# Kernel optimization log

Measured on AMD Instinct MI355X. Metric: run time of the kernel, lower is better.

Reference implementation:

```python
import jax, jax.numpy as jnp
import numpy as np


def setup_inputs() -> dict:
    key = jax.random.key(0)
    ks = jax.random.split(key, 5)
    B, H, S, D = 4, 16, 2048, 64
    queries = jax.random.normal(ks[0], (B, H, S, D), dtype=jnp.float32)
    keys = jax.random.normal(ks[1], (B, H, S, D), dtype=jnp.float32)
    values = jax.random.normal(ks[2], (B, H, S, D), dtype=jnp.float32)
    W_out = jax.random.normal(ks[3], (D, D), dtype=jnp.float32) / np.sqrt(D)
    b_out = jax.random.normal(ks[4], (D,), dtype=jnp.float32) * 0.01
    return {"queries": queries, "keys": keys, "values": values, "W_out": W_out, "b_out": b_out}


def reference(queries, keys, values, W_out, b_out):
    # scores: [B,H,S,S] = Q K^T / sqrt(D)
    scale = 1.0 / np.sqrt(queries.shape[-1]).astype(np.float32)
    scores = jnp.einsum("bhqd,bhkd->bhqk", queries, keys) * scale
    # concrete attention distribution: softmax over keys axis
    distr = jax.nn.softmax(scores, axis=-1)
    # weighted sum of values: [B,H,S,D]
    out = jnp.einsum("bhqk,bhkd->bhqd", distr, values)
    # out projection (nn.Linear: x @ W^T + b)
    out = jnp.einsum("bhqd,ed->bhqe", out, W_out) + b_out
    return out
```

## Files before the change

kernel.cpp:

```cpp
#include <hip/hip_runtime.h>
#include <math.h>


typedef __attribute__((ext_vector_type(8)))  short    s16x8;
typedef __attribute__((ext_vector_type(4)))  float    f32x4;
typedef __attribute__((ext_vector_type(16))) float    f32x16;
typedef __attribute__((ext_vector_type(4)))  unsigned u32x4;

#define KQSCALE 0.18033688011112042f

__device__ __forceinline__ unsigned short f2bu(float x) {
    __bf16 v = (__bf16)x;
    return __builtin_bit_cast(unsigned short, v);
}
__device__ __forceinline__ short f2b(float x) { return (short)f2bu(x); }
__device__ __forceinline__ float b2f(short s) {
    __bf16 v = __builtin_bit_cast(__bf16, (unsigned short)s);
    return (float)v;
}
__device__ __forceinline__ unsigned pack2(float lo, float hi) {
    return (unsigned)f2bu(lo) | ((unsigned)f2bu(hi) << 16);
}
__device__ __forceinline__ int swzK(int row) { return (row & 7) << 4; }
__device__ __forceinline__ int swzV(int row) { return (((row >> 4) & 3) ^ (row & 7)) << 4; }

#define PLSWAP(x, y) asm("v_permlane32_swap_b32 %0, %1" : "+v"(x), "+v"(y))

#define BARRIER()                                              \
    do {                                                       \
        asm volatile("s_waitcnt lgkmcnt(0)" ::: "memory");     \
        __builtin_amdgcn_s_barrier();                          \
    } while (0)

#define WAVE_LDS_FENCE()                                       \
    do {                                                       \
        asm volatile("s_waitcnt lgkmcnt(0)" ::: "memory");     \
        __builtin_amdgcn_sched_barrier(0);                     \
    } while (0)

#define QK2(SA, SB, KsC, KT)                                                    \
    f32x16 SA = {}; f32x16 SB = {};                                             \
    __builtin_amdgcn_s_setprio(1);                                              \
    _Pragma("unroll")                                                           \
    for (int dt = 0; dt < 4; ++dt) {                                            \
        const int krow = (KT) * 32 + q32;                                       \
        s16x8 kf = *(s16x8*)((KsC) + krow * 128 +                               \
                             ((dt * 32 + h * 16) ^ swzK(krow)));                \
        SA = __builtin_amdgcn_mfma_f32_32x32x16_bf16(kf, qfA[dt], SA, 0, 0, 0); \
        SB = __builtin_amdgcn_mfma_f32_32x32x16_bf16(kf, qfB[dt], SB, 0, 0, 0); \
    }                                                                           \
    __builtin_amdgcn_s_setprio(0);

#define PVQ2(SA, SB, VtC, KT, T)                                               \
    do {                                                                       \
        const float ea0 = __builtin_amdgcn_exp2f((SA)[8 * (T) + 0]);           \
        const float ea1 = __builtin_amdgcn_exp2f((SA)[8 * (T) + 1]);           \
        const float ea2 = __builtin_amdgcn_exp2f((SA)[8 * (T) + 2]);           \
        const float ea3 = __builtin_amdgcn_exp2f((SA)[8 * (T) + 3]);           \
        const float ea4 = __builtin_amdgcn_exp2f((SA)[8 * (T) + 4]);           \
        const float ea5 = __builtin_amdgcn_exp2f((SA)[8 * (T) + 5]);           \
        const float ea6 = __builtin_amdgcn_exp2f((SA)[8 * (T) + 6]);           \
        const float ea7 = __builtin_amdgcn_exp2f((SA)[8 * (T) + 7]);           \
        const float eb0 = __builtin_amdgcn_exp2f((SB)[8 * (T) + 0]);           \
        const float eb1 = __builtin_amdgcn_exp2f((SB)[8 * (T) + 1]);           \
        const float eb2 = __builtin_amdgcn_exp2f((SB)[8 * (T) + 2]);           \
        const float eb3 = __builtin_amdgcn_exp2f((SB)[8 * (T) + 3]);           \
        const float eb4 = __builtin_amdgcn_exp2f((SB)[8 * (T) + 4]);           \
        const float eb5 = __builtin_amdgcn_exp2f((SB)[8 * (T) + 5]);           \
        const float eb6 = __builtin_amdgcn_exp2f((SB)[8 * (T) + 6]);           \
        const float eb7 = __builtin_amdgcn_exp2f((SB)[8 * (T) + 7]);           \
        unsigned ka0 = pack2(ea0, ea1), ka1 = pack2(ea2, ea3);                 \
        unsigned ka2 = pack2(ea4, ea5), ka3 = pack2(ea6, ea7);                 \
        PLSWAP(ka0, ka2);                                                      \
        PLSWAP(ka1, ka3);                                                      \
        u32x4 pwA; pwA[0] = ka0; pwA[1] = ka1; pwA[2] = ka2; pwA[3] = ka3;     \
        const s16x8 pA_ = __builtin_bit_cast(s16x8, pwA);                      \
        unsigned kb0 = pack2(eb0, eb1), kb1 = pack2(eb2, eb3);                 \
        unsigned kb2 = pack2(eb4, eb5), kb3 = pack2(eb6, eb7);                 \
        PLSWAP(kb0, kb2);                                                      \
        PLSWAP(kb1, kb3);                                                      \
        u32x4 pwB; pwB[0] = kb0; pwB[1] = kb1; pwB[2] = kb2; pwB[3] = kb3;     \
        const s16x8 pB_ = __builtin_bit_cast(s16x8, pwB);                      \
        const int kbo = (KT) * 64 + (T) * 32 + h * 16;                         \
        __builtin_amdgcn_s_setprio(1);                                         \
        s16x8 vf0 = *(s16x8*)((VtC) + q32 * 128 + (kbo ^ swzV(q32)));          \
        s16x8 vf1 = *(s16x8*)((VtC) + (32 + q32) * 128 + (kbo ^ swzV(32 + q32))); \
        accA0 = __builtin_amdgcn_mfma_f32_32x32x16_bf16(pA_, vf0, accA0, 0, 0, 0); \
        accB0 = __builtin_amdgcn_mfma_f32_32x32x16_bf16(pB_, vf0, accB0, 0, 0, 0); \
        accA1 = __builtin_amdgcn_mfma_f32_32x32x16_bf16(pA_, vf1, accA1, 0, 0, 0); \
        accB1 = __builtin_amdgcn_mfma_f32_32x32x16_bf16(pB_, vf1, accB1, 0, 0, 0); \
        rsA = __builtin_amdgcn_mfma_f32_32x32x16_bf16(pA_, onesV, rsA, 0, 0, 0); \
        rsB = __builtin_amdgcn_mfma_f32_32x32x16_bf16(pB_, onesV, rsB, 0, 0, 0); \
        __builtin_amdgcn_s_setprio(0);                                         \
    } while (0)

__global__ __launch_bounds__(512) void attn_fused(
    const float* __restrict__ Qg, const float* __restrict__ Kg,
    const float* __restrict__ Vg, const float* __restrict__ Wg,
    const float* __restrict__ bg, float* __restrict__ outg)
{
    __shared__ __align__(16) char smem[65536];
    char* KsB0 = smem;
    char* VtB0 = smem + 8192;
    char* KsB1 = smem + 16384;
    char* VtB1 = smem + 24576;
    char* KsB2 = smem + 32768;
    char* VtB2 = smem + 40960;
    char* KsB3 = smem + 49152;
    char* VtB3 = smem + 57344;

    const int tid  = threadIdx.x;
    const int wave = tid >> 6;
    const int lane = tid & 63;
    const int h    = lane >> 5;
    const int q32  = lane & 31;
    const int g    = lane >> 4;
    const int c    = lane & 15;

    const int orig = blockIdx.x;
    const int wg   = (orig & 7) * 32 + (orig >> 3);
    const int bh   = wg >> 2;
    const int qblk = wg & 3;

    const float* Qh = Qg + (size_t)bh * (2048 * 64);
    const float* Kh = Kg + (size_t)bh * (2048 * 64);
    const float* Vh = Vg + (size_t)bh * (2048 * 64);
    float*       Oh = outg + (size_t)bh * (2048 * 64);

    const int qbaseA = qblk * 512 + wave * 32;
    const int qbaseB = qbaseA + 256;

    const int srow = tid >> 3;
    const int scb  = (tid & 7) * 8;
    const int vk   = (tid >> 4) * 2;
    const int vd4  = (tid & 15) * 4;
    const int kOff = srow * 64 + scb;
    const int vOff = vk * 64 + vd4;

    f32x4 qLa[4], qLb[4], qLc[4], qLd[4];
#pragma unroll
    for (int dt = 0; dt < 4; ++dt) {
        const float* sA = Qh + (size_t)(qbaseA + q32) * 64 + dt * 16 + h * 8;
        const float* sB = Qh + (size_t)(qbaseB + q32) * 64 + dt * 16 + h * 8;
        qLa[dt] = *(const f32x4*)(sA);
        qLb[dt] = *(const f32x4*)(sA + 4);
        qLc[dt] = *(const f32x4*)(sB);
        qLd[dt] = *(const f32x4*)(sB + 4);
    }

    f32x4 rK0, rK1;
    f32x4 rV0, rV1;

    auto issueK = [&](int chunk) {
        const float* p = Kh + (size_t)chunk * 4096 + kOff;
        rK0 = *(const f32x4*)(p);
        rK1 = *(const f32x4*)(p + 4);
    };
    auto issueV = [&](int chunk) {
        const float* p = Vh + (size_t)chunk * 4096 + vOff;
        rV0 = *(const f32x4*)(p);
        rV1 = *(const f32x4*)(p + 64);
    };
    auto stageK = [&](char* KsD) {
        u32x4 wA;
        wA[0] = pack2(rK0[0], rK0[1]); wA[1] = pack2(rK0[2], rK0[3]);
        wA[2] = pack2(rK1[0], rK1[1]); wA[3] = pack2(rK1[2], rK1[3]);
        *(u32x4*)(KsD + srow * 128 + ((scb * 2) ^ swzK(srow))) = wA;
    };
    auto stageV = [&](char* VtD) {
#pragma unroll
        for (int i = 0; i < 4; ++i) {
            const int d = vd4 + i;
            *(unsigned*)(VtD + d * 128 + ((2 * vk) ^ swzV(d))) = pack2(rV0[i], rV1[i]);
        }
    };

    s16x8 qfA[4], qfB[4];
#pragma unroll
    for (int dt = 0; dt < 4; ++dt) {
        u32x4 fA, fB;
        fA[0] = pack2(qLa[dt][0] * KQSCALE, qLa[dt][1] * KQSCALE);
        fA[1] = pack2(qLa[dt][2] * KQSCALE, qLa[dt][3] * KQSCALE);
        fA[2] = pack2(qLb[dt][0] * KQSCALE, qLb[dt][1] * KQSCALE);
        fA[3] = pack2(qLb[dt][2] * KQSCALE, qLb[dt][3] * KQSCALE);
        fB[0] = pack2(qLc[dt][0] * KQSCALE, qLc[dt][1] * KQSCALE);
        fB[1] = pack2(qLc[dt][2] * KQSCALE, qLc[dt][3] * KQSCALE);
        fB[2] = pack2(qLd[dt][0] * KQSCALE, qLd[dt][1] * KQSCALE);
        fB[3] = pack2(qLd[dt][2] * KQSCALE, qLd[dt][3] * KQSCALE);
        qfA[dt] = __builtin_bit_cast(s16x8, fA);
        qfB[dt] = __builtin_bit_cast(s16x8, fB);
    }

    f32x16 accA0 = {}, accA1 = {}, accB0 = {}, accB1 = {};
    f32x16 rsA = {}, rsB = {};
    u32x4 onesW;
    onesW[0] = 0x3F803F80u; onesW[1] = 0x3F803F80u;
    onesW[2] = 0x3F803F80u; onesW[3] = 0x3F803F80u;
    const s16x8 onesV = __builtin_bit_cast(s16x8, onesW);

    auto one_iter = [&](char* KsC, char* VtC, char* KsS, char* VtS, int kc) {
        QK2(s0A, s0B, KsC, 0);
        PVQ2(s0A, s0B, VtC, 0, 0);
        if (kc <= 29) {
            stageK(KsS);
            if (kc <= 28) issueK(kc + 3);
        }
        PVQ2(s0A, s0B, VtC, 0, 1);
        QK2(s1A, s1B, KsC, 1);
        PVQ2(s1A, s1B, VtC, 1, 0);
        if (kc <= 29) {
            stageV(VtS);
            if (kc <= 28) issueV(kc + 3);
        }
        PVQ2(s1A, s1B, VtC, 1, 1);
    };

    issueK(0); issueV(0);
    stageK(KsB0); stageV(VtB0);
    issueK(1); issueV(1);
    stageK(KsB1); stageV(VtB1);
    issueK(2); issueV(2);
    BARRIER();

    for (int kc = 0; kc < 32; kc += 4) {
        one_iter(KsB0, VtB0, KsB2, VtB2, kc);
        one_iter(KsB1, VtB1, KsB3, VtB3, kc + 1);
        BARRIER();
        one_iter(KsB2, VtB2, KsB0, VtB0, kc + 2);
        one_iter(KsB3, VtB3, KsB1, VtB1, kc + 3);
        BARRIER();
    }

#pragma unroll
    for (int r = 0; r < 16; ++r) {
        const float ivA = __builtin_amdgcn_rcpf(rsA[r]);
        const float ivB = __builtin_amdgcn_rcpf(rsB[r]);
        accA0[r] *= ivA;  accA1[r] *= ivA;
        accB0[r] *= ivB;  accB1[r] *= ivB;
    }

    auto stageO = [&](const f32x16& a0, const f32x16& a1) {
        char* Ow = smem + wave * 8192;
#pragma unroll
        for (int r = 0; r < 16; ++r) {
            const int row = (r & 3) + 8 * (r >> 2) + 4 * h;
            const int sw  = (row & 7) << 5;
            *(float*)(Ow + row * 256 + ((q32 * 4)       ^ sw)) = a0[r];
            *(float*)(Ow + row * 256 + ((128 + q32 * 4) ^ sw)) = a1[r];
        }
    };
    auto project = [&](int qb) {
        char* Ow = smem + wave * 8192;
        f32x4 po[2][4];
#pragma unroll
        for (int rt = 0; rt < 2; ++rt)
#pragma unroll
            for (int et = 0; et < 4; ++et) {
                po[rt][et][0] = 0.f; po[rt][et][1] = 0.f;
                po[rt][et][2] = 0.f; po[rt][et][3] = 0.f;
            }
#pragma unroll
        for (int kh = 0; kh < 2; ++kh) {
            s16x8 ahi[2], alo[2];
#pragma unroll
            for (int rt = 0; rt < 2; ++rt) {
                const int row = rt * 16 + c;
                const int rb  = row * 256;
                const int rsw = (row & 7) << 5;
                const int o0  = (kh * 128 + g * 32) ^ rsw;
                f32x4 x0 = *(f32x4*)(Ow + rb + o0);
                f32x4 x1 = *(f32x4*)(Ow + rb + o0 + 16);
                s16x8 hh8, lo8;
#pragma unroll
                for (int j = 0; j < 4; ++j) {
                    const short hv = f2b(x0[j]);
                    hh8[j] = hv;  lo8[j] = f2b(x0[j] - b2f(hv));
                }
#pragma unroll
                for (int j = 0; j < 4; ++j) {
                    const short hv = f2b(x1[j]);
                    hh8[4 + j] = hv;  lo8[4 + j] = f2b(x1[j] - b2f(hv));
                }
                ahi[rt] = hh8; alo[rt] = lo8;
            }
#pragma unroll
            for (int et = 0; et < 4; ++et) {
                const float* ws = Wg + (et * 16 + c) * 64 + kh * 32 + g * 8;
                f32x4 w0 = *(const f32x4*)ws;
                f32x4 w1 = *(const f32x4*)(ws + 4);
                s16x8 whi, wlo;
#pragma unroll
                for (int j = 0; j < 4; ++j) {
                    const short hv = f2b(w0[j]);
                    whi[j] = hv;  wlo[j] = f2b(w0[j] - b2f(hv));
                }
#pragma unroll
                for (int j = 0; j < 4; ++j) {
                    const short hv = f2b(w1[j]);
                    whi[4 + j] = hv;  wlo[4 + j] = f2b(w1[j] - b2f(hv));
                }
#pragma unroll
                for (int rt = 0; rt < 2; ++rt) {
                    po[rt][et] = __builtin_amdgcn_mfma_f32_16x16x32_bf16(ahi[rt], whi, po[rt][et], 0, 0, 0);
                    po[rt][et] = __builtin_amdgcn_mfma_f32_16x16x32_bf16(alo[rt], whi, po[rt][et], 0, 0, 0);
                    po[rt][et] = __builtin_amdgcn_mfma_f32_16x16x32_bf16(ahi[rt], wlo, po[rt][et], 0, 0, 0);
                }
            }
        }
#pragma unroll
        for (int et = 0; et < 4; ++et) {
            const float bb = bg[et * 16 + c];
#pragma unroll
            for (int rt = 0; rt < 2; ++rt)
#pragma unroll
                for (int r = 0; r < 4; ++r) {
                    const int qrow = qb + rt * 16 + 4 * g + r;
                    Oh[(size_t)qrow * 64 + et * 16 + c] = po[rt][et][r] + bb;
                }
        }
    };

    stageO(accA0, accA1);
    WAVE_LDS_FENCE();
    project(qbaseA);
    WAVE_LDS_FENCE();
    stageO(accB0, accB1);
    WAVE_LDS_FENCE();
    project(qbaseB);
}

extern "C" void kernel_launch(void* const* d_in, const int* in_sizes, int n_in,
                              void* d_out, int out_size, void* d_ws, size_t ws_size,
                              hipStream_t stream) {
    const float* Q = (const float*)d_in[0];
    const float* K = (const float*)d_in[1];
    const float* V = (const float*)d_in[2];
    const float* W = (const float*)d_in[3];
    const float* b = (const float*)d_in[4];
    float* out = (float*)d_out;
    hipLaunchKernelGGL(attn_fused, dim3(256), dim3(512), 0, stream, Q, K, V, W, b, out);
}
```

Measured before the change: 94.16 us.

## Split key range across wave halves and double grid with LDS partial reduction

Waves are split into two groups that each process half of every K/V chunk for the same query tiles. The grid doubles to 512 blocks, each covering 256 queries instead of 512. Partial outputs and row sums are then combined through shared memory before normalization and the output projection. This trades more K/V traffic and extra barriers and LDS reduction work for more blocks and shorter per-wave dependency chains.

```diff
diff --git a/kernel.cpp b/kernel.cpp
--- a/kernel.cpp
+++ b/kernel.cpp
@@ -117,18 +117,21 @@
     const int g    = lane >> 4;
     const int c    = lane & 15;
 
+    const int khalf = wave >> 2;
+    const int qt    = wave & 3;
+
     const int orig = blockIdx.x;
-    const int wg   = (orig & 7) * 32 + (orig >> 3);
-    const int bh   = wg >> 2;
-    const int qblk = wg & 3;
+    const int wg   = (orig & 7) * 64 + (orig >> 3);
+    const int bh   = wg >> 3;
+    const int qblk = wg & 7;
 
     const float* Qh = Qg + (size_t)bh * (2048 * 64);
     const float* Kh = Kg + (size_t)bh * (2048 * 64);
     const float* Vh = Vg + (size_t)bh * (2048 * 64);
     float*       Oh = outg + (size_t)bh * (2048 * 64);
 
-    const int qbaseA = qblk * 512 + wave * 32;
-    const int qbaseB = qbaseA + 256;
+    const int qbaseA = qblk * 256 + qt * 32;
+    const int qbaseB = qbaseA + 128;
 
     const int srow = tid >> 3;
     const int scb  = (tid & 7) * 8;
@@ -199,20 +202,17 @@
     const s16x8 onesV = __builtin_bit_cast(s16x8, onesW);
 
     auto one_iter = [&](char* KsC, char* VtC, char* KsS, char* VtS, int kc) {
-        QK2(s0A, s0B, KsC, 0);
-        PVQ2(s0A, s0B, VtC, 0, 0);
+        QK2(sA, sB, KsC, khalf);
+        PVQ2(sA, sB, VtC, khalf, 0);
         if (kc <= 29) {
             stageK(KsS);
             if (kc <= 28) issueK(kc + 3);
         }
-        PVQ2(s0A, s0B, VtC, 0, 1);
-        QK2(s1A, s1B, KsC, 1);
-        PVQ2(s1A, s1B, VtC, 1, 0);
+        PVQ2(sA, sB, VtC, khalf, 1);
         if (kc <= 29) {
             stageV(VtS);
             if (kc <= 28) issueV(kc + 3);
         }
-        PVQ2(s1A, s1B, VtC, 1, 1);
     };
 
     issueK(0); issueV(0);
@@ -231,26 +231,47 @@
         BARRIER();
     }
 
-#pragma unroll
-    for (int r = 0; r < 16; ++r) {
-        const float ivA = __builtin_amdgcn_rcpf(rsA[r]);
-        const float ivB = __builtin_amdgcn_rcpf(rsB[r]);
-        accA0[r] *= ivA;  accA1[r] *= ivA;
-        accB0[r] *= ivB;  accB1[r] *= ivB;
-    }
+    char* OwSelf = smem + wave * 8192;
+    char* OwPart = smem + (wave ^ 4) * 8192;
 
     auto stageO = [&](const f32x16& a0, const f32x16& a1) {
-        char* Ow = smem + wave * 8192;
 #pragma unroll
         for (int r = 0; r < 16; ++r) {
             const int row = (r & 3) + 8 * (r >> 2) + 4 * h;
             const int sw  = (row & 7) << 5;
-            *(float*)(Ow + row * 256 + ((q32 * 4)       ^ sw)) = a0[r];
-            *(float*)(Ow + row * 256 + ((128 + q32 * 4) ^ sw)) = a1[r];
+            *(float*)(OwSelf + row * 256 + ((q32 * 4)       ^ sw)) = a0[r];
+            *(float*)(OwSelf + row * 256 + ((128 + q32 * 4) ^ sw)) = a1[r];
+        }
+    };
+    auto stageRS = [&](char* dst, const f32x16& rsv) {
+        if (q32 == 0) {
+#pragma unroll
+            for (int r = 0; r < 16; ++r) {
+                const int row = (r & 3) + 8 * (r >> 2) + 4 * h;
+                *(float*)(dst + row * 4) = rsv[r];
+            }
+        }
+    };
+    auto reduceO = [&](const f32x16& a0, const f32x16& a1, const f32x16& rsv,
+                       char* rsbuf) {
+        float iv[16];
+#pragma unroll
+        for (int r = 0; r < 16; ++r) {
+            const int row = (r & 3) + 8 * (r >> 2) + 4 * h;
+            iv[r] = __builtin_amdgcn_rcpf(rsv[r] + *(float*)(rsbuf + row * 4));
+        }
+        __builtin_amdgcn_sched_barrier(0);
+#pragma unroll
+        for (int r = 0; r < 16; ++r) {
+            const int row = (r & 3) + 8 * (r >> 2) + 4 * h;
+            const int sw  = (row & 7) << 5;
+            const float p0 = *(float*)(OwPart + row * 256 + ((q32 * 4)       ^ sw));
+            const float p1 = *(float*)(OwPart + row * 256 + ((128 + q32 * 4) ^ sw));
+            *(float*)(OwSelf + row * 256 + ((q32 * 4)       ^ sw)) = (a0[r] + p0) * iv[r];
+            *(float*)(OwSelf + row * 256 + ((128 + q32 * 4) ^ sw)) = (a1[r] + p1) * iv[r];
         }
     };
     auto project = [&](int qb) {
-        char* Ow = smem + wave * 8192;
         f32x4 po[2][4];
 #pragma unroll
         for (int rt = 0; rt < 2; ++rt)
@@ -268,8 +289,8 @@
                 const int rb  = row * 256;
                 const int rsw = (row & 7) << 5;
                 const int o0  = (kh * 128 + g * 32) ^ rsw;
-                f32x4 x0 = *(f32x4*)(Ow + rb + o0);
-                f32x4 x1 = *(f32x4*)(Ow + rb + o0 + 16);
+                f32x4 x0 = *(f32x4*)(OwSelf + rb + o0);
+                f32x4 x1 = *(f32x4*)(OwSelf + rb + o0 + 16);
                 s16x8 hh8, lo8;
 #pragma unroll
                 for (int j = 0; j < 4; ++j) {
@@ -320,13 +341,28 @@
         }
     };
 
-    stageO(accA0, accA1);
-    WAVE_LDS_FENCE();
-    project(qbaseA);
-    WAVE_LDS_FENCE();
-    stageO(accB0, accB1);
-    WAVE_LDS_FENCE();
-    project(qbaseB);
+    if (khalf == 1) {
+        stageO(accA0, accA1);
+        stageRS(smem + qt * 8192, rsA);
+    }
+    BARRIER();
+    if (khalf == 0) {
+        reduceO(accA0, accA1, rsA, smem + qt * 8192);
+        WAVE_LDS_FENCE();
+        project(qbaseA);
+    }
+    BARRIER();
+
+    if (khalf == 0) {
+        stageO(accB0, accB1);
+        stageRS(smem + (4 + qt) * 8192, rsB);
+    }
+    BARRIER();
+    if (khalf == 1) {
+        reduceO(accB0, accB1, rsB, smem + wave * 8192);
+        WAVE_LDS_FENCE();
+        project(qbaseB);
+    }
 }
 
 extern "C" void kernel_launch(void* const* d_in, const int* in_sizes, int n_in,
@@ -338,5 +374,5 @@
     const float* W = (const float*)d_in[3];
     const float* b = (const float*)d_in[4];
     float* out = (float*)d_out;
-    hipLaunchKernelGGL(attn_fused, dim3(256), dim3(512), 0, stream, Q, K, V, W, b, out);
-}
+    hipLaunchKernelGGL(attn_fused, dim3(512), dim3(512), 0, stream, Q, K, V, W, b, out);
+}
```

Measured after the change: 112.8 us. +19.8%, slower.
